# Optimization experiments

Hardware: AMD Instinct MI355X
Metric: run time of the kernel (lower is better)

Reference implementation:

```python
import jax, jax.numpy as jnp
import numpy as np

B, T, D, H = 4, 1024, 1024, 16
NUM_BUCKETS = 320
MAX_DIST = 800
LN_EPS = 1e-5


def _rel_bucket(T):
    # bidirectional T5-style relative position buckets
    ctx = jnp.arange(T)[:, None]
    mem = jnp.arange(T)[None, :]
    rel = mem - ctx  # (T, T)
    half = NUM_BUCKETS // 2  # 160
    bucket = (rel > 0).astype(jnp.int32) * half
    n = jnp.abs(rel)
    max_exact = half // 2  # 80
    is_small = n < max_exact
    n_f = jnp.maximum(n, 1).astype(jnp.float32)
    large = max_exact + (
        jnp.log(n_f / max_exact) / np.log(MAX_DIST / max_exact) * (half - max_exact)
    ).astype(jnp.int32)
    large = jnp.minimum(large, half - 1)
    return bucket + jnp.where(is_small, n, large)


def setup_inputs() -> dict:
    key = jax.random.key(0)
    ks = jax.random.split(key, 12)
    s = 0.02
    return {
        "x": jax.random.normal(ks[0], (B, T, D), jnp.float32),
        "ln_w": jnp.ones((D,), jnp.float32),
        "ln_b": jnp.zeros((D,), jnp.float32),
        "wq": jax.random.normal(ks[1], (D, D), jnp.float32) * s,
        "bq": jnp.zeros((D,), jnp.float32),
        "wk": jax.random.normal(ks[2], (D, D), jnp.float32) * s,
        "bk": jnp.zeros((D,), jnp.float32),
        "wv": jax.random.normal(ks[3], (D, D), jnp.float32) * s,
        "bv": jnp.zeros((D,), jnp.float32),
        "wo": jax.random.normal(ks[4], (D, D), jnp.float32) * s,
        "bo": jnp.zeros((D,), jnp.float32),
        "rel_emb": jax.random.normal(ks[5], (NUM_BUCKETS, H), jnp.float32) * s,
        "grep_w": jax.random.normal(ks[6], (8, D // H), jnp.float32) * s,
        "grep_b": jnp.zeros((8,), jnp.float32),
        "grep_a": jnp.ones((1, H, 1, 1), jnp.float32),
    }


def reference(x, ln_w, ln_b, wq, bq, wk, bk, wv, bv, wo, bo, rel_emb, grep_w, grep_b, grep_a):
    Bb, Tt, Dd = x.shape
    hd = Dd // H
    scaling = hd ** -0.5
    # pre-norm LayerNorm
    mu = jnp.mean(x, -1, keepdims=True)
    var = jnp.mean((x - mu) ** 2, -1, keepdims=True)
    h = (x - mu) / jnp.sqrt(var + LN_EPS) * ln_w + ln_b
    # projections (q pre-scaled as in fairseq/WavLM)
    q = (h @ wq.T + bq) * scaling
    k = h @ wk.T + bk
    v = h @ wv.T + bv
    q = q.reshape(Bb, Tt, H, hd).transpose(0, 2, 1, 3)  # (B,H,T,hd)
    k = k.reshape(Bb, Tt, H, hd).transpose(0, 2, 1, 3)
    v = v.reshape(Bb, Tt, H, hd).transpose(0, 2, 1, 3)
    # bucketed relative position bias: (H, T, T)
    buckets = _rel_bucket(Tt)
    pos_bias = rel_emb[buckets].transpose(2, 0, 1)
    # gru_rel_pos gating (per batch, head, query position)
    alpha = 32.0
    ql = q * (alpha / scaling)  # undo scaling, multiply by alpha
    g = jax.nn.sigmoid((ql @ grep_w.T + grep_b).reshape(Bb, H, Tt, 2, 4).sum(-1))
    gate_a, gate_b = g[..., 0:1], g[..., 1:2]  # (B,H,T,1)
    gate = gate_a * (gate_b * grep_a - 1.0) + 2.0
    # attention
    scores = jnp.einsum('bhtd,bhsd->bhts', q, k) + gate * pos_bias[None]
    attn = jax.nn.softmax(scores, axis=-1)
    out = jnp.einsum('bhts,bhsd->bhtd', attn, v).transpose(0, 2, 1, 3).reshape(Bb, Tt, Dd)
    # output projection, dropout (identity in eval), residual
    out = out @ wo.T + bo + x
    pos_bias_out = jnp.broadcast_to(pos_bias[None], (Bb, H, Tt, Tt)).reshape(Bb * H, Tt, Tt)
    return out, pos_bias_out
```

## Files before the change

kernel.cpp:

```cpp
#include <hip/hip_runtime.h>

typedef unsigned short u16;
typedef __attribute__((ext_vector_type(8))) short short8;
typedef __attribute__((ext_vector_type(4))) float floatx4;

#define MFMA16(a, b, c) __builtin_amdgcn_mfma_f32_16x16x32_bf16(a, b, c, 0, 0, 0)

__device__ __forceinline__ float bf2f(u16 u) {
  return __uint_as_float(((unsigned int)u) << 16);
}
__device__ __forceinline__ u16 f2bf(float f) {
  unsigned int u = __float_as_uint(f);
  unsigned int r = (u + 0x7fffu + ((u >> 16) & 1u)) >> 16;
  return (u16)r;
}

__global__ __launch_bounds__(256) void ln_kernel(
    const float* __restrict__ x, const float* __restrict__ w, const float* __restrict__ bb,
    u16* __restrict__ hb)
{
  int wid = threadIdx.x >> 6, lane = threadIdx.x & 63;
  int row = blockIdx.x * 4 + wid;
  const float* xr = x + row * 1024 + lane * 16;
  float xs[16];
#pragma unroll
  for (int i = 0; i < 4; i++) {
    float4 v = *(const float4*)(xr + i * 4);
    xs[i * 4 + 0] = v.x; xs[i * 4 + 1] = v.y; xs[i * 4 + 2] = v.z; xs[i * 4 + 3] = v.w;
  }
  float s = 0.f, ss = 0.f;
#pragma unroll
  for (int i = 0; i < 16; i++) { s += xs[i]; ss += xs[i] * xs[i]; }
#pragma unroll
  for (int m = 1; m < 64; m <<= 1) { s += __shfl_xor(s, m, 64); ss += __shfl_xor(ss, m, 64); }
  float mu = s * (1.0f / 1024.0f);
  float var = ss * (1.0f / 1024.0f) - mu * mu;
  float rstd = rsqrtf(var + 1e-5f);
  const float* wr = w + lane * 16;
  const float* br = bb + lane * 16;
  short8 o0, o1;
#pragma unroll
  for (int i = 0; i < 8; i++) {
    o0[i] = (short)f2bf((xs[i] - mu) * rstd * wr[i] + br[i]);
    o1[i] = (short)f2bf((xs[8 + i] - mu) * rstd * wr[8 + i] + br[8 + i]);
  }
  u16* hr = hb + row * 1024 + lane * 16;
  *(short8*)hr = o0;
  *(short8*)(hr + 8) = o1;
}

__global__ __launch_bounds__(256) void convw_kernel(
    const float* __restrict__ wq, const float* __restrict__ wk,
    const float* __restrict__ wv, const float* __restrict__ wo,
    u16* __restrict__ wb)
{
  int idx = (blockIdx.x * 256 + threadIdx.x) * 8;
  int seg = idx >> 20, off = idx & 1048575;
  const float* s = (seg == 0) ? wq : (seg == 1) ? wk : (seg == 2) ? wv : wo;
  float4 f0 = *(const float4*)(s + off);
  float4 f1 = *(const float4*)(s + off + 4);
  short8 o;
  o[0] = (short)f2bf(f0.x); o[1] = (short)f2bf(f0.y);
  o[2] = (short)f2bf(f0.z); o[3] = (short)f2bf(f0.w);
  o[4] = (short)f2bf(f1.x); o[5] = (short)f2bf(f1.y);
  o[6] = (short)f2bf(f1.z); o[7] = (short)f2bf(f1.w);
  *(short8*)&wb[idx] = o;
}

__global__ __launch_bounds__(256) void qkv_kernel(
    const u16* __restrict__ hb, const u16* __restrict__ wb,
    const float* __restrict__ bq, const float* __restrict__ bk, const float* __restrict__ bv,
    u16* __restrict__ qs, u16* __restrict__ kko, u16* __restrict__ vt)
{
  __shared__ u16 As[128 * 32];
  __shared__ u16 Bs[128 * 32];
  int tid = threadIdx.x;
  int wid = tid >> 6, lane = tid & 63;
  int wm = wid >> 1, wn = wid & 1;
  int l15 = lane & 15, quad = lane >> 4;
  int m0 = blockIdx.y * 128;
  int n0g = blockIdx.x * 128;
  int sec = n0g >> 10;
  int n0 = n0g & 1023;
  const u16* W = wb + sec * 1048576;
  const float* bias = (sec == 0) ? bq : ((sec == 1) ? bk : bv);

  floatx4 zero4 = {0.f, 0.f, 0.f, 0.f};
  floatx4 acc[4][4];
#pragma unroll
  for (int i = 0; i < 4; i++)
#pragma unroll
    for (int j = 0; j < 4; j++) acc[i][j] = zero4;

  int lr = tid >> 2;
  int lc = (tid & 3) * 8;

  for (int kt = 0; kt < 1024; kt += 32) {
    *(short8*)&As[lr * 32 + lc]        = *(const short8*)&hb[(m0 + lr) * 1024 + kt + lc];
    *(short8*)&As[(lr + 64) * 32 + lc] = *(const short8*)&hb[(m0 + lr + 64) * 1024 + kt + lc];
    *(short8*)&Bs[lr * 32 + lc]        = *(const short8*)&W[(n0 + lr) * 1024 + kt + lc];
    *(short8*)&Bs[(lr + 64) * 32 + lc] = *(const short8*)&W[(n0 + lr + 64) * 1024 + kt + lc];
    __syncthreads();
    short8 af[4], bf[4];
#pragma unroll
    for (int mi = 0; mi < 4; mi++)
      af[mi] = *(const short8*)&As[(wm * 64 + mi * 16 + l15) * 32 + quad * 8];
#pragma unroll
    for (int ni = 0; ni < 4; ni++)
      bf[ni] = *(const short8*)&Bs[(wn * 64 + ni * 16 + l15) * 32 + quad * 8];
#pragma unroll
    for (int mi = 0; mi < 4; mi++)
#pragma unroll
      for (int ni = 0; ni < 4; ni++)
        acc[mi][ni] = MFMA16(af[mi], bf[ni], acc[mi][ni]);
    __syncthreads();
  }

  int bidx = m0 >> 10;
#pragma unroll
  for (int mi = 0; mi < 4; mi++) {
#pragma unroll
    for (int ni = 0; ni < 4; ni++) {
#pragma unroll
      for (int r = 0; r < 4; r++) {
        int row = m0 + wm * 64 + mi * 16 + quad * 4 + r;
        int t = row & 1023;
        int c = n0 + wn * 64 + ni * 16 + l15;
        float val = acc[mi][ni][r] + bias[c];
        int hh = c >> 6, hp = c & 63;
        if (sec == 0) {
          val *= 0.125f;
          qs[((bidx * 16 + hh) * 1024 + t) * 64 + hp] = f2bf(val);
        } else if (sec == 1) {
          kko[((bidx * 16 + hh) * 1024 + t) * 64 + hp] = f2bf(val);
        } else {
          vt[((bidx * 16 + hh) * 64 + hp) * 1024 + t] = f2bf(val);
        }
      }
    }
  }
}

__device__ __forceinline__ int rel_bucket(int t, int s) {
  int rel = s - t;
  int bucket = (rel > 0) ? 160 : 0;
  int n = (rel < 0) ? -rel : rel;
  if (n < 80) return bucket + n;
  float a = logf((float)n / 80.0f);
  float c = a / (float)2.302585092994046;
  float v = c * 80.0f;
  int large = 80 + (int)v;
  if (large > 159) large = 159;
  return bucket + large;
}

__global__ __launch_bounds__(256) void bias0_kernel(
    const float* __restrict__ rel_emb, float* __restrict__ out1)
{
  int tid = blockIdx.x * 256 + threadIdx.x;
  int t = tid >> 7;
  int s0 = (tid & 127) * 8;
  int bkt[8];
#pragma unroll
  for (int j = 0; j < 8; j++) bkt[j] = rel_bucket(t, s0 + j) * 16;
  int base_ts = t * 1024 + s0;
#pragma unroll
  for (int hh = 0; hh < 16; hh++) {
    float4 v0, v1;
    v0.x = rel_emb[bkt[0] + hh]; v0.y = rel_emb[bkt[1] + hh];
    v0.z = rel_emb[bkt[2] + hh]; v0.w = rel_emb[bkt[3] + hh];
    v1.x = rel_emb[bkt[4] + hh]; v1.y = rel_emb[bkt[5] + hh];
    v1.z = rel_emb[bkt[6] + hh]; v1.w = rel_emb[bkt[7] + hh];
    float* p = out1 + hh * 1048576 + base_ts;
    *(float4*)p = v0;
    *(float4*)(p + 4) = v1;
  }
}

__global__ __launch_bounds__(256) void bias_copy_kernel(float* __restrict__ out1)
{
  int idx = blockIdx.x * 256 + threadIdx.x;
  float4 v = *(const float4*)&out1[idx * 4];
  *(float4*)&out1[16777216 + idx * 4] = v;
  *(float4*)&out1[33554432 + idx * 4] = v;
  *(float4*)&out1[50331648 + idx * 4] = v;
}

__global__ __launch_bounds__(256) void attn_kernel(
    const u16* __restrict__ qs, const u16* __restrict__ kko, const u16* __restrict__ vt,
    const float* __restrict__ gw, const float* __restrict__ gb, const float* __restrict__ ga,
    const float* __restrict__ bias, u16* __restrict__ ao)
{
  __shared__ __align__(16) u16 Pb[4][16 * 32];
  int wid = threadIdx.x >> 6, lane = threadIdx.x & 63;
  int l15 = lane & 15, quad = lane >> 4;
  int bh = blockIdx.x;
  int b = bh >> 4, h = bh & 15;
  int q0 = blockIdx.y * 64 + wid * 16;
  const u16* Q = qs + bh * 65536;
  const u16* K = kko + bh * 65536;
  const u16* V = vt + bh * 65536;
  const float* Bi = bias + h * 1048576;
  u16* pb = &Pb[wid][0];

  const u16* qrow = Q + (q0 + l15) * 64;
  float e[8];
#pragma unroll
  for (int i = 0; i < 8; i++) e[i] = gb[i];
  for (int j = 0; j < 64; j++) {
    float ql = bf2f(qrow[j]) * 256.0f;
#pragma unroll
    for (int i = 0; i < 8; i++) e[i] += ql * gw[i * 64 + j];
  }
  float u0 = e[0] + e[1] + e[2] + e[3];
  float u1 = e[4] + e[5] + e[6] + e[7];
  float sa = 1.0f / (1.0f + __expf(-u0));
  float sb = 1.0f / (1.0f + __expf(-u1));
  float gv = sa * (sb * ga[h] - 1.0f) + 2.0f;

  short8 qf0 = *(const short8*)&Q[(q0 + l15) * 64 + quad * 8];
  short8 qf1 = *(const short8*)&Q[(q0 + l15) * 64 + quad * 8 + 32];
  float gt[4], mrun[4], lrun[4];
#pragma unroll
  for (int r = 0; r < 4; r++) {
    gt[r] = __shfl(gv, quad * 4 + r, 64);
    mrun[r] = -1e30f;
    lrun[r] = 0.f;
  }
  floatx4 zero4 = {0.f, 0.f, 0.f, 0.f};
  floatx4 accO[4];
#pragma unroll
  for (int ni = 0; ni < 4; ni++) accO[ni] = zero4;

  for (int s0 = 0; s0 < 1024; s0 += 32) {
    floatx4 sc0 = zero4, sc1 = zero4;
    short8 kf;
    kf = *(const short8*)&K[(s0 + l15) * 64 + quad * 8];
    sc0 = MFMA16(qf0, kf, sc0);
    kf = *(const short8*)&K[(s0 + l15) * 64 + quad * 8 + 32];
    sc0 = MFMA16(qf1, kf, sc0);
    kf = *(const short8*)&K[(s0 + 16 + l15) * 64 + quad * 8];
    sc1 = MFMA16(qf0, kf, sc1);
    kf = *(const short8*)&K[(s0 + 16 + l15) * 64 + quad * 8 + 32];
    sc1 = MFMA16(qf1, kf, sc1);

#pragma unroll
    for (int r = 0; r < 4; r++) {
      int t = q0 + quad * 4 + r;
      float v0 = sc0[r] + gt[r] * Bi[t * 1024 + s0 + l15];
      float v1 = sc1[r] + gt[r] * Bi[t * 1024 + s0 + 16 + l15];
      float mt = fmaxf(v0, v1);
#pragma unroll
      for (int m = 1; m < 16; m <<= 1) mt = fmaxf(mt, __shfl_xor(mt, m, 64));
      float mnew = fmaxf(mrun[r], mt);
      float alpha = __expf(fmaxf(mrun[r] - mnew, -80.0f));
      float p0 = __expf(v0 - mnew);
      float p1 = __expf(v1 - mnew);
      float ps = p0 + p1;
#pragma unroll
      for (int m = 1; m < 16; m <<= 1) ps += __shfl_xor(ps, m, 64);
      lrun[r] = lrun[r] * alpha + ps;
      mrun[r] = mnew;
#pragma unroll
      for (int ni = 0; ni < 4; ni++) accO[ni][r] *= alpha;
      pb[(quad * 4 + r) * 32 + l15] = f2bf(p0);
      pb[(quad * 4 + r) * 32 + 16 + l15] = f2bf(p1);
    }
    __syncthreads();
    short8 pf = *(const short8*)&pb[l15 * 32 + quad * 8];
#pragma unroll
    for (int ni = 0; ni < 4; ni++) {
      short8 vf = *(const short8*)&V[(ni * 16 + l15) * 1024 + s0 + quad * 8];
      accO[ni] = MFMA16(pf, vf, accO[ni]);
    }
  }
#pragma unroll
  for (int ni = 0; ni < 4; ni++) {
#pragma unroll
    for (int r = 0; r < 4; r++) {
      int t = q0 + quad * 4 + r;
      float val = accO[ni][r] / lrun[r];
      ao[(b * 1024 + t) * 1024 + h * 64 + ni * 16 + l15] = f2bf(val);
    }
  }
}

__global__ __launch_bounds__(256) void oproj_kernel(
    const u16* __restrict__ ao, const u16* __restrict__ wob, const float* __restrict__ bo,
    const float* __restrict__ x, float* __restrict__ out)
{
  __shared__ u16 As[128 * 32];
  __shared__ u16 Bs[128 * 32];
  int tid = threadIdx.x;
  int wid = tid >> 6, lane = tid & 63;
  int wm = wid >> 1, wn = wid & 1;
  int l15 = lane & 15, quad = lane >> 4;
  int m0 = blockIdx.y * 128;
  int n0 = blockIdx.x * 128;

  floatx4 zero4 = {0.f, 0.f, 0.f, 0.f};
  floatx4 acc[4][4];
#pragma unroll
  for (int i = 0; i < 4; i++)
#pragma unroll
    for (int j = 0; j < 4; j++) acc[i][j] = zero4;

  int lr = tid >> 2;
  int lc = (tid & 3) * 8;

  for (int kt = 0; kt < 1024; kt += 32) {
    *(short8*)&As[lr * 32 + lc]        = *(const short8*)&ao[(m0 + lr) * 1024 + kt + lc];
    *(short8*)&As[(lr + 64) * 32 + lc] = *(const short8*)&ao[(m0 + lr + 64) * 1024 + kt + lc];
    *(short8*)&Bs[lr * 32 + lc]        = *(const short8*)&wob[(n0 + lr) * 1024 + kt + lc];
    *(short8*)&Bs[(lr + 64) * 32 + lc] = *(const short8*)&wob[(n0 + lr + 64) * 1024 + kt + lc];
    __syncthreads();
    short8 af[4], bf[4];
#pragma unroll
    for (int mi = 0; mi < 4; mi++)
      af[mi] = *(const short8*)&As[(wm * 64 + mi * 16 + l15) * 32 + quad * 8];
#pragma unroll
    for (int ni = 0; ni < 4; ni++)
      bf[ni] = *(const short8*)&Bs[(wn * 64 + ni * 16 + l15) * 32 + quad * 8];
#pragma unroll
    for (int mi = 0; mi < 4; mi++)
#pragma unroll
      for (int ni = 0; ni < 4; ni++)
        acc[mi][ni] = MFMA16(af[mi], bf[ni], acc[mi][ni]);
    __syncthreads();
  }

#pragma unroll
  for (int mi = 0; mi < 4; mi++) {
#pragma unroll
    for (int ni = 0; ni < 4; ni++) {
#pragma unroll
      for (int r = 0; r < 4; r++) {
        int row = m0 + wm * 64 + mi * 16 + quad * 4 + r;
        int c = n0 + wn * 64 + ni * 16 + l15;
        out[row * 1024 + c] = acc[mi][ni][r] + bo[c] + x[row * 1024 + c];
      }
    }
  }
}

extern "C" void kernel_launch(void* const* d_in, const int* in_sizes, int n_in,
                              void* d_out, int out_size, void* d_ws, size_t ws_size,
                              hipStream_t stream) {
  const float* x    = (const float*)d_in[0];
  const float* ln_w = (const float*)d_in[1];
  const float* ln_b = (const float*)d_in[2];
  const float* wq   = (const float*)d_in[3];
  const float* bq   = (const float*)d_in[4];
  const float* wk   = (const float*)d_in[5];
  const float* bk   = (const float*)d_in[6];
  const float* wv   = (const float*)d_in[7];
  const float* bv   = (const float*)d_in[8];
  const float* wo   = (const float*)d_in[9];
  const float* bo   = (const float*)d_in[10];
  const float* rel  = (const float*)d_in[11];
  const float* gw   = (const float*)d_in[12];
  const float* gb   = (const float*)d_in[13];
  const float* ga   = (const float*)d_in[14];

  float* out0  = (float*)d_out;
  float* out1f = out0 + 4194304;

  u16* hbb = (u16*)(out1f + 16777216);
  u16* wbb = (u16*)(out1f + 18874368);
  u16* qsb = (u16*)(out1f + 20971520);
  u16* kkb = (u16*)(out1f + 23068672);
  u16* vtb = (u16*)(out1f + 25165824);
  u16* aob = (u16*)(out1f + 27262976);

  ln_kernel<<<1024, 256, 0, stream>>>(x, ln_w, ln_b, hbb);
  convw_kernel<<<2048, 256, 0, stream>>>(wq, wk, wv, wo, wbb);
  qkv_kernel<<<dim3(24, 32), 256, 0, stream>>>(hbb, wbb, bq, bk, bv, qsb, kkb, vtb);
  bias0_kernel<<<512, 256, 0, stream>>>(rel, out1f);
  attn_kernel<<<dim3(64, 16), 256, 0, stream>>>(qsb, kkb, vtb, gw, gb, ga, out1f, aob);
  oproj_kernel<<<dim3(8, 32), 256, 0, stream>>>(aob, wbb + 3145728, bo, x, out0);
  bias_copy_kernel<<<16384, 256, 0, stream>>>(out1f);
}
```

Measured before the change: 537.6 us.

## Use compact relative-bias table in attention and fuse bias output writes

Attention now reads the position bias from a small per-head table indexed by relative offset (s - t), replacing reads of the full T×T bias tensor. It also computes the score transpose so each lane holds a query column, software-prefetches the next K tile and bias values, double-buffers the P tile in shared memory, and packs the bf16 conversion into one instruction. V is written row-major by the QKV projection and transposed by a separate LDS kernel. The bias output is written to all four batch copies in a single kernel, removing the read-back copy pass. The cost is two extra small kernels and some added register pressure in the attention loop.

Result: no change. 533.4 us (-0.8%).

```diff
diff --git a/kernel.cpp b/kernel.cpp
--- a/kernel.cpp
+++ b/kernel.cpp
@@ -67,10 +67,36 @@
   *(short8*)&wb[idx] = o;
 }
 
+__device__ __forceinline__ int rel_bucket(int t, int s) {
+  int rel = s - t;
+  int bucket = (rel > 0) ? 160 : 0;
+  int n = (rel < 0) ? -rel : rel;
+  if (n < 80) return bucket + n;
+  float a = logf((float)n / 80.0f);
+  float c = a / (float)2.302585092994046;
+  float v = c * 80.0f;
+  int large = 80 + (int)v;
+  if (large > 159) large = 159;
+  return bucket + large;
+}
+
+__global__ __launch_bounds__(256) void bias_table_kernel(
+    const float* __restrict__ rel_emb, float* __restrict__ tbl)
+{
+  int idx = blockIdx.x * 256 + threadIdx.x;
+  int h = idx & 15, ri = idx >> 4;
+  float v = 0.f;
+  if (ri < 2047) {
+    int rel = ri - 1023;
+    v = rel_emb[rel_bucket(0, rel) * 16 + h];
+  }
+  tbl[h * 2048 + ri] = v;
+}
+
 __global__ __launch_bounds__(256) void qkv_kernel(
     const u16* __restrict__ hb, const u16* __restrict__ wb,
     const float* __restrict__ bq, const float* __restrict__ bk, const float* __restrict__ bv,
-    u16* __restrict__ qs, u16* __restrict__ kko, u16* __restrict__ vt)
+    u16* __restrict__ qs, u16* __restrict__ kko, u16* __restrict__ vn)
 {
   __shared__ u16 As[128 * 32];
   __shared__ u16 Bs[128 * 32];
@@ -134,64 +160,43 @@
         } else if (sec == 1) {
           kko[((bidx * 16 + hh) * 1024 + t) * 64 + hp] = f2bf(val);
         } else {
-          vt[((bidx * 16 + hh) * 64 + hp) * 1024 + t] = f2bf(val);
+          vn[((bidx * 16 + hh) * 1024 + t) * 64 + hp] = f2bf(val);
         }
       }
     }
   }
 }
 
-__device__ __forceinline__ int rel_bucket(int t, int s) {
-  int rel = s - t;
-  int bucket = (rel > 0) ? 160 : 0;
-  int n = (rel < 0) ? -rel : rel;
-  if (n < 80) return bucket + n;
-  float a = logf((float)n / 80.0f);
-  float c = a / (float)2.302585092994046;
-  float v = c * 80.0f;
-  int large = 80 + (int)v;
-  if (large > 159) large = 159;
-  return bucket + large;
-}
-
-__global__ __launch_bounds__(256) void bias0_kernel(
-    const float* __restrict__ rel_emb, float* __restrict__ out1)
-{
-  int tid = blockIdx.x * 256 + threadIdx.x;
-  int t = tid >> 7;
-  int s0 = (tid & 127) * 8;
-  int bkt[8];
-#pragma unroll
-  for (int j = 0; j < 8; j++) bkt[j] = rel_bucket(t, s0 + j) * 16;
-  int base_ts = t * 1024 + s0;
-#pragma unroll
-  for (int hh = 0; hh < 16; hh++) {
-    float4 v0, v1;
-    v0.x = rel_emb[bkt[0] + hh]; v0.y = rel_emb[bkt[1] + hh];
-    v0.z = rel_emb[bkt[2] + hh]; v0.w = rel_emb[bkt[3] + hh];
-    v1.x = rel_emb[bkt[4] + hh]; v1.y = rel_emb[bkt[5] + hh];
-    v1.z = rel_emb[bkt[6] + hh]; v1.w = rel_emb[bkt[7] + hh];
-    float* p = out1 + hh * 1048576 + base_ts;
-    *(float4*)p = v0;
-    *(float4*)(p + 4) = v1;
-  }
-}
-
-__global__ __launch_bounds__(256) void bias_copy_kernel(float* __restrict__ out1)
-{
-  int idx = blockIdx.x * 256 + threadIdx.x;
-  float4 v = *(const float4*)&out1[idx * 4];
-  *(float4*)&out1[16777216 + idx * 4] = v;
-  *(float4*)&out1[33554432 + idx * 4] = v;
-  *(float4*)&out1[50331648 + idx * 4] = v;
+__global__ __launch_bounds__(256) void vtrans_kernel(
+    const u16* __restrict__ vn, u16* __restrict__ vt)
+{
+  __shared__ u16 Ts[64 * 72];
+  int bh = blockIdx.x >> 4;
+  int t0 = (blockIdx.x & 15) * 64;
+  int tid = threadIdx.x;
+  int row = tid >> 2;
+  int c16 = (tid & 3) * 16;
+  const u16* src = vn + bh * 65536 + (t0 + row) * 64 + c16;
+  *(short8*)&Ts[row * 72 + c16]     = *(const short8*)&src[0];
+  *(short8*)&Ts[row * 72 + c16 + 8] = *(const short8*)&src[8];
+  __syncthreads();
+  short8 o0, o1;
+#pragma unroll
+  for (int j = 0; j < 8; j++) {
+    o0[j] = (short)Ts[(c16 + j) * 72 + row];
+    o1[j] = (short)Ts[(c16 + 8 + j) * 72 + row];
+  }
+  u16* dst = vt + bh * 65536 + row * 1024 + t0 + c16;
+  *(short8*)&dst[0] = o0;
+  *(short8*)&dst[8] = o1;
 }
 
 __global__ __launch_bounds__(256) void attn_kernel(
     const u16* __restrict__ qs, const u16* __restrict__ kko, const u16* __restrict__ vt,
     const float* __restrict__ gw, const float* __restrict__ gb, const float* __restrict__ ga,
-    const float* __restrict__ bias, u16* __restrict__ ao)
-{
-  __shared__ __align__(16) u16 Pb[4][16 * 32];
+    const float* __restrict__ tbl, u16* __restrict__ ao)
+{
+  __shared__ __align__(16) u16 Pb[4][2 * 768];
   int wid = threadIdx.x >> 6, lane = threadIdx.x & 63;
   int l15 = lane & 15, quad = lane >> 4;
   int bh = blockIdx.x;
@@ -200,87 +205,142 @@
   const u16* Q = qs + bh * 65536;
   const u16* K = kko + bh * 65536;
   const u16* V = vt + bh * 65536;
-  const float* Bi = bias + h * 1048576;
-  u16* pb = &Pb[wid][0];
+  u16* pbase = &Pb[wid][0];
 
   const u16* qrow = Q + (q0 + l15) * 64;
   float e[8];
 #pragma unroll
-  for (int i = 0; i < 8; i++) e[i] = gb[i];
-  for (int j = 0; j < 64; j++) {
-    float ql = bf2f(qrow[j]) * 256.0f;
-#pragma unroll
-    for (int i = 0; i < 8; i++) e[i] += ql * gw[i * 64 + j];
-  }
-  float u0 = e[0] + e[1] + e[2] + e[3];
-  float u1 = e[4] + e[5] + e[6] + e[7];
+  for (int i = 0; i < 8; i++) e[i] = 0.f;
+  {
+    short8 qa = *(const short8*)&qrow[quad * 16];
+    short8 qc = *(const short8*)&qrow[quad * 16 + 8];
+#pragma unroll
+    for (int jj = 0; jj < 8; jj++) {
+      float qla = bf2f((u16)qa[jj]) * 256.0f;
+      float qlb = bf2f((u16)qc[jj]) * 256.0f;
+      int j = quad * 16 + jj;
+#pragma unroll
+      for (int i = 0; i < 8; i++) {
+        e[i] += qla * gw[i * 64 + j];
+        e[i] += qlb * gw[i * 64 + j + 8];
+      }
+    }
+  }
+#pragma unroll
+  for (int i = 0; i < 8; i++) {
+    e[i] += __shfl_xor(e[i], 16, 64);
+    e[i] += __shfl_xor(e[i], 32, 64);
+  }
+  float u0 = e[0] + e[1] + e[2] + e[3] + gb[0] + gb[1] + gb[2] + gb[3];
+  float u1 = e[4] + e[5] + e[6] + e[7] + gb[4] + gb[5] + gb[6] + gb[7];
   float sa = 1.0f / (1.0f + __expf(-u0));
-  float sb = 1.0f / (1.0f + __expf(-u1));
-  float gv = sa * (sb * ga[h] - 1.0f) + 2.0f;
+  float sc_ = 1.0f / (1.0f + __expf(-u1));
+  float gv = sa * (sc_ * ga[h] - 1.0f) + 2.0f;
 
   short8 qf0 = *(const short8*)&Q[(q0 + l15) * 64 + quad * 8];
   short8 qf1 = *(const short8*)&Q[(q0 + l15) * 64 + quad * 8 + 32];
-  float gt[4], mrun[4], lrun[4];
-#pragma unroll
-  for (int r = 0; r < 4; r++) {
-    gt[r] = __shfl(gv, quad * 4 + r, 64);
-    mrun[r] = -1e30f;
-    lrun[r] = 0.f;
-  }
+
+  const float* tb = tbl + h * 2048 + 1023 + quad * 4 - (q0 + l15);
+
+  float mrun = -1e30f, lrun = 0.f;
   floatx4 zero4 = {0.f, 0.f, 0.f, 0.f};
   floatx4 accO[4];
 #pragma unroll
   for (int ni = 0; ni < 4; ni++) accO[ni] = zero4;
 
-  for (int s0 = 0; s0 < 1024; s0 += 32) {
+  const u16* Kr = K + l15 * 64 + quad * 8;
+  short8 ka0 = *(const short8*)&Kr[0];
+  short8 ka1 = *(const short8*)&Kr[32];
+  short8 kb0 = *(const short8*)&Kr[16 * 64];
+  short8 kb1 = *(const short8*)&Kr[16 * 64 + 32];
+  float bt[8];
+#pragma unroll
+  for (int r = 0; r < 4; r++) { bt[r] = tb[r]; bt[4 + r] = tb[16 + r]; }
+
+  for (int it = 0; it < 32; it++) {
+    int s0 = it * 32;
     floatx4 sc0 = zero4, sc1 = zero4;
-    short8 kf;
-    kf = *(const short8*)&K[(s0 + l15) * 64 + quad * 8];
-    sc0 = MFMA16(qf0, kf, sc0);
-    kf = *(const short8*)&K[(s0 + l15) * 64 + quad * 8 + 32];
-    sc0 = MFMA16(qf1, kf, sc0);
-    kf = *(const short8*)&K[(s0 + 16 + l15) * 64 + quad * 8];
-    sc1 = MFMA16(qf0, kf, sc1);
-    kf = *(const short8*)&K[(s0 + 16 + l15) * 64 + quad * 8 + 32];
-    sc1 = MFMA16(qf1, kf, sc1);
-
+    sc0 = MFMA16(ka0, qf0, sc0);
+    sc0 = MFMA16(ka1, qf1, sc0);
+    sc1 = MFMA16(kb0, qf0, sc1);
+    sc1 = MFMA16(kb1, qf1, sc1);
+
+    int sn = (s0 + 32) & 1023;
+    const u16* Kn = K + (sn + l15) * 64 + quad * 8;
+    short8 na0 = *(const short8*)&Kn[0];
+    short8 na1 = *(const short8*)&Kn[32];
+    short8 nb0 = *(const short8*)&Kn[16 * 64];
+    short8 nb1 = *(const short8*)&Kn[16 * 64 + 32];
+    float btn[8];
+#pragma unroll
+    for (int r = 0; r < 4; r++) { btn[r] = tb[sn + r]; btn[4 + r] = tb[sn + 16 + r]; }
+    short8 vf0 = *(const short8*)&V[(0 * 16 + l15) * 1024 + s0 + quad * 8];
+    short8 vf1 = *(const short8*)&V[(1 * 16 + l15) * 1024 + s0 + quad * 8];
+    short8 vf2 = *(const short8*)&V[(2 * 16 + l15) * 1024 + s0 + quad * 8];
+    short8 vf3 = *(const short8*)&V[(3 * 16 + l15) * 1024 + s0 + quad * 8];
+
+    float vv[8];
 #pragma unroll
     for (int r = 0; r < 4; r++) {
-      int t = q0 + quad * 4 + r;
-      float v0 = sc0[r] + gt[r] * Bi[t * 1024 + s0 + l15];
-      float v1 = sc1[r] + gt[r] * Bi[t * 1024 + s0 + 16 + l15];
-      float mt = fmaxf(v0, v1);
-#pragma unroll
-      for (int m = 1; m < 16; m <<= 1) mt = fmaxf(mt, __shfl_xor(mt, m, 64));
-      float mnew = fmaxf(mrun[r], mt);
-      float alpha = __expf(fmaxf(mrun[r] - mnew, -80.0f));
-      float p0 = __expf(v0 - mnew);
-      float p1 = __expf(v1 - mnew);
-      float ps = p0 + p1;
-#pragma unroll
-      for (int m = 1; m < 16; m <<= 1) ps += __shfl_xor(ps, m, 64);
-      lrun[r] = lrun[r] * alpha + ps;
-      mrun[r] = mnew;
-#pragma unroll
-      for (int ni = 0; ni < 4; ni++) accO[ni][r] *= alpha;
-      pb[(quad * 4 + r) * 32 + l15] = f2bf(p0);
-      pb[(quad * 4 + r) * 32 + 16 + l15] = f2bf(p1);
-    }
-    __syncthreads();
-    short8 pf = *(const short8*)&pb[l15 * 32 + quad * 8];
+      vv[r]     = sc0[r] + gv * bt[r];
+      vv[4 + r] = sc1[r] + gv * bt[4 + r];
+    }
+    float mt = fmaxf(fmaxf(fmaxf(vv[0], vv[1]), fmaxf(vv[2], vv[3])),
+                     fmaxf(fmaxf(vv[4], vv[5]), fmaxf(vv[6], vv[7])));
+    mt = fmaxf(mt, __shfl_xor(mt, 16, 64));
+    mt = fmaxf(mt, __shfl_xor(mt, 32, 64));
+    float mnew = fmaxf(mrun, mt);
+    float al = __expf(fmaxf(mrun - mnew, -80.0f));
+    float p[8], ps = 0.f;
+#pragma unroll
+    for (int j = 0; j < 8; j++) { p[j] = __expf(vv[j] - mnew); ps += p[j]; }
+    ps += __shfl_xor(ps, 16, 64);
+    ps += __shfl_xor(ps, 32, 64);
+    lrun = lrun * al + ps;
+    mrun = mnew;
+
+    float ar[4];
+#pragma unroll
+    for (int r = 0; r < 4; r++) ar[r] = __shfl(al, quad * 4 + r, 64);
 #pragma unroll
     for (int ni = 0; ni < 4; ni++) {
-      short8 vf = *(const short8*)&V[(ni * 16 + l15) * 1024 + s0 + quad * 8];
-      accO[ni] = MFMA16(pf, vf, accO[ni]);
-    }
-  }
-#pragma unroll
-  for (int ni = 0; ni < 4; ni++) {
-#pragma unroll
-    for (int r = 0; r < 4; r++) {
-      int t = q0 + quad * 4 + r;
-      float val = accO[ni][r] / lrun[r];
-      ao[(b * 1024 + t) * 1024 + h * 64 + ni * 16 + l15] = f2bf(val);
+      floatx4 t = accO[ni];
+      t[0] *= ar[0]; t[1] *= ar[1]; t[2] *= ar[2]; t[3] *= ar[3];
+      accO[ni] = t;
+    }
+
+    unsigned w0, w1, w2, w3;
+    asm("v_cvt_pk_bf16_f32 %0, %1, %2" : "=v"(w0) : "v"(p[0]), "v"(p[1]));
+    asm("v_cvt_pk_bf16_f32 %0, %1, %2" : "=v"(w1) : "v"(p[2]), "v"(p[3]));
+    asm("v_cvt_pk_bf16_f32 %0, %1, %2" : "=v"(w2) : "v"(p[4]), "v"(p[5]));
+    asm("v_cvt_pk_bf16_f32 %0, %1, %2" : "=v"(w3) : "v"(p[6]), "v"(p[7]));
+    u16* pw = pbase + (it & 1) * 768;
+    uint2 wa; wa.x = w0; wa.y = w1;
+    uint2 wbv; wbv.x = w2; wbv.y = w3;
+    *(uint2*)&pw[l15 * 48 + quad * 4] = wa;
+    *(uint2*)&pw[l15 * 48 + 16 + quad * 4] = wbv;
+    asm volatile("s_waitcnt lgkmcnt(0)" ::: "memory");
+    __builtin_amdgcn_sched_barrier(0);
+    short8 pf = *(const short8*)&pw[l15 * 48 + quad * 8];
+
+    accO[0] = MFMA16(pf, vf0, accO[0]);
+    accO[1] = MFMA16(pf, vf1, accO[1]);
+    accO[2] = MFMA16(pf, vf2, accO[2]);
+    accO[3] = MFMA16(pf, vf3, accO[3]);
+
+    ka0 = na0; ka1 = na1; kb0 = nb0; kb1 = nb1;
+#pragma unroll
+    for (int j = 0; j < 8; j++) bt[j] = btn[j];
+  }
+
+#pragma unroll
+  for (int r = 0; r < 4; r++) {
+    float lr = __shfl(lrun, quad * 4 + r, 64);
+    float rl = 1.0f / lr;
+    int t = q0 + quad * 4 + r;
+#pragma unroll
+    for (int ni = 0; ni < 4; ni++) {
+      ao[(b * 1024 + t) * 1024 + h * 64 + ni * 16 + l15] = f2bf(accO[ni][r] * rl);
     }
   }
 }
@@ -340,6 +400,31 @@
         out[row * 1024 + c] = acc[mi][ni][r] + bo[c] + x[row * 1024 + c];
       }
     }
+  }
+}
+
+__global__ __launch_bounds__(256) void bias_all_kernel(
+    const float* __restrict__ rel_emb, float* __restrict__ out1)
+{
+  int tid = blockIdx.x * 256 + threadIdx.x;
+  int t = tid >> 7;
+  int s0 = (tid & 127) * 8;
+  int bkt[8];
+#pragma unroll
+  for (int j = 0; j < 8; j++) bkt[j] = rel_bucket(t, s0 + j) * 16;
+  int base_ts = t * 1024 + s0;
+#pragma unroll
+  for (int hh = 0; hh < 16; hh++) {
+    float4 v0, v1;
+    v0.x = rel_emb[bkt[0] + hh]; v0.y = rel_emb[bkt[1] + hh];
+    v0.z = rel_emb[bkt[2] + hh]; v0.w = rel_emb[bkt[3] + hh];
+    v1.x = rel_emb[bkt[4] + hh]; v1.y = rel_emb[bkt[5] + hh];
+    v1.z = rel_emb[bkt[6] + hh]; v1.w = rel_emb[bkt[7] + hh];
+    float* p = out1 + hh * 1048576 + base_ts;
+    *(float4*)p = v0;              *(float4*)(p + 4) = v1;
+    *(float4*)(p + 16777216) = v0; *(float4*)(p + 16777216 + 4) = v1;
+    *(float4*)(p + 33554432) = v0; *(float4*)(p + 33554432 + 4) = v1;
+    *(float4*)(p + 50331648) = v0; *(float4*)(p + 50331648 + 4) = v1;
   }
 }
 
@@ -365,18 +450,21 @@
   float* out0  = (float*)d_out;
   float* out1f = out0 + 4194304;
 
-  u16* hbb = (u16*)(out1f + 16777216);
-  u16* wbb = (u16*)(out1f + 18874368);
-  u16* qsb = (u16*)(out1f + 20971520);
-  u16* kkb = (u16*)(out1f + 23068672);
-  u16* vtb = (u16*)(out1f + 25165824);
-  u16* aob = (u16*)(out1f + 27262976);
+  u16* hbb  = (u16*)(out1f + 16777216);
+  u16* wbb  = (u16*)(out1f + 18874368);
+  u16* qsb  = (u16*)(out1f + 20971520);
+  u16* kkb  = (u16*)(out1f + 23068672);
+  u16* vnb  = (u16*)(out1f + 25165824);
+  u16* vtb  = (u16*)(out1f + 27262976);
+  u16* aob  = (u16*)(out1f + 29360128);
+  float* tbl =        out1f + 31457280;
 
   ln_kernel<<<1024, 256, 0, stream>>>(x, ln_w, ln_b, hbb);
   convw_kernel<<<2048, 256, 0, stream>>>(wq, wk, wv, wo, wbb);
-  qkv_kernel<<<dim3(24, 32), 256, 0, stream>>>(hbb, wbb, bq, bk, bv, qsb, kkb, vtb);
-  bias0_kernel<<<512, 256, 0, stream>>>(rel, out1f);
-  attn_kernel<<<dim3(64, 16), 256, 0, stream>>>(qsb, kkb, vtb, gw, gb, ga, out1f, aob);
+  bias_table_kernel<<<128, 256, 0, stream>>>(rel, tbl);
+  qkv_kernel<<<dim3(24, 32), 256, 0, stream>>>(hbb, wbb, bq, bk, bv, qsb, kkb, vnb);
+  vtrans_kernel<<<1024, 256, 0, stream>>>(vnb, vtb);
+  attn_kernel<<<dim3(64, 16), 256, 0, stream>>>(qsb, kkb, vtb, gw, gb, ga, tbl, aob);
   oproj_kernel<<<dim3(8, 32), 256, 0, stream>>>(aob, wbb + 3145728, bo, x, out0);
-  bias_copy_kernel<<<16384, 256, 0, stream>>>(out1f);
-}
+  bias_all_kernel<<<512, 256, 0, stream>>>(rel, out1f);
+}
```
